# Kernel tuning notes

Hardware: AMD Instinct MI355X
Metric: run time of the kernel (lower is better)

Reference implementation:

```python
import jax, jax.numpy as jnp
import numpy as np

TEMP = 1.0
EPS = 1e-8
DIM = 1024
CODEBOOK_SIZE = 8192
N = 8192


def setup_inputs() -> dict:
    key = jax.random.key(0)
    k_h, k_cb, k_w, k_b = jax.random.split(key, 4)
    h = jax.random.normal(k_h, (N, DIM), dtype=jnp.float32)
    codebook = jax.random.normal(k_cb, (CODEBOOK_SIZE, DIM), dtype=jnp.float32)
    # RMSNorm scale initialized to ones (as in the torch module)
    scale = jnp.ones((DIM,), dtype=jnp.float32)
    # nn.Linear(dim, dim): weight [out, in], bias [out]
    bound = 1.0 / np.sqrt(DIM)
    W = jax.random.uniform(k_w, (DIM, DIM), dtype=jnp.float32, minval=-bound, maxval=bound)
    b = jax.random.uniform(k_b, (DIM,), dtype=jnp.float32, minval=-bound, maxval=bound)
    return {"h": h, "codebook": codebook, "scale": scale, "W": W, "b": b}


def reference(h, codebook, scale, W, b):
    # Squared distances via GEMM identity: ||h-c||^2 = ||h||^2 + ||c||^2 - 2 h.c
    h_sq = jnp.sum(h * h, axis=-1, keepdims=True)              # [N, 1]
    c_sq = jnp.sum(codebook * codebook, axis=-1)               # [K]
    dist = h_sq + c_sq[None, :] - 2.0 * (h @ codebook.T)       # [N, K]
    q = jax.nn.softmax(-dist / TEMP, axis=-1)                  # [N, K]
    z_e = q @ codebook                                         # [N, D]
    # residual MLP: RMSNorm then Linear
    r = h - z_e
    rms = jnp.sqrt(jnp.mean(r * r, axis=-1, keepdims=True))
    x = r / (rms + EPS) * scale
    z_q = z_e + x @ W.T + b
    return z_q
```

## Files before the change

kernel.cpp:

```cpp
#include <hip/hip_runtime.h>

typedef unsigned short u16;
typedef unsigned char u8;
typedef signed char s8;
typedef __attribute__((ext_vector_type(8))) short bf16x8;
typedef __attribute__((ext_vector_type(4))) float f32x4;
typedef __attribute__((ext_vector_type(4))) int i32x4;

__device__ __forceinline__ u16 f2bf(float x) {
  unsigned int u = __float_as_uint(x);
  u = u + 0x7FFFu + ((u >> 16) & 1u);
  return (u16)(u >> 16);
}
__device__ __forceinline__ float bf2f(u16 v) {
  return __uint_as_float(((unsigned int)v) << 16);
}

typedef const __attribute__((address_space(1))) void gas_void;
typedef __attribute__((address_space(3))) void las_void;

__device__ __forceinline__ void gld_lds16(const void* g, void* l) {
  __builtin_amdgcn_global_load_lds((gas_void*)g, (las_void*)l, 16, 0, 0);
}

#define BM 128
#define BN 128
#define BK 64
#define CAP 512
#define DU8 14

__global__ __launch_bounds__(256) void gemm_c8(
    const s8* __restrict__ A0, const s8* __restrict__ B0,
    u8* __restrict__ S, const float* __restrict__ c_sq) {
  __shared__ __align__(16) s8 lA[128 * 128];
  __shared__ __align__(16) s8 lB[128 * 128];
  int tid = threadIdx.x, wave = tid >> 6, lane = tid & 63;
  long bm = (long)blockIdx.y * 128, bn = (long)blockIdx.x * 128;
  int wm = (wave >> 1) * 64, wn = (wave & 1) * 64;
  int r15 = lane & 15, kg = lane >> 4;
  int srow = wave * 8 + (lane >> 3);
  int scol = ((lane & 7) ^ (lane >> 3)) * 16;

  i32x4 acc[4][4];
#pragma unroll
  for (int i = 0; i < 4; ++i)
#pragma unroll
    for (int j = 0; j < 4; ++j) acc[i][j] = (i32x4){0, 0, 0, 0};

  const s8* ap = A0 + bm * 1024;
  const s8* bp = B0 + bn * 1024;

  for (int k0 = 0; k0 < 1024; k0 += 128) {
    __syncthreads();
#pragma unroll
    for (int c = 0; c < 4; ++c) {
      long go = (long)(c * 32 + srow) * 1024 + k0 + scol;
      int ldoff = c * 4096 + wave * 1024;
      gld_lds16(ap + go, lA + ldoff);
      gld_lds16(bp + go, lB + ldoff);
    }
    __syncthreads();
#pragma unroll
    for (int kk = 0; kk < 2; ++kk) {
      int cb = ((kk * 4 + kg) ^ (r15 & 7)) * 16;
      i32x4 bf[4];
#pragma unroll
      for (int j = 0; j < 4; ++j)
        bf[j] = *(const i32x4*)&lB[(wn + j * 16 + r15) * 128 + cb];
#pragma unroll
      for (int i = 0; i < 4; ++i) {
        i32x4 af = *(const i32x4*)&lA[(wm + i * 16 + r15) * 128 + cb];
#pragma unroll
        for (int j = 0; j < 4; ++j)
          acc[i][j] = __builtin_amdgcn_mfma_i32_16x16x64_i8(af, bf[j], acc[i][j], 0, 0, 0);
      }
    }
  }

#pragma unroll
  for (int i = 0; i < 4; ++i) {
    long rg = bm + wm + i * 16 + kg * 4;
#pragma unroll
    for (int j = 0; j < 4; ++j) {
      long cg = bn + wn + j * 16 + r15;
      float csq = c_sq[cg];
      i32x4 m = acc[i][j];
#pragma unroll
      for (int r = 0; r < 4; ++r) {
        float v = csq - (float)m[r] * 0.0078125f;
        int q = (int)rintf((v - 1024.f) * 0.25f) + 128;
        q = q < 0 ? 0 : (q > 255 ? 255 : q);
        S[(rg + r) * 8192 + cg] = (u8)q;
      }
    }
  }
}

__device__ __forceinline__ void stage_tile(const u16* __restrict__ src, long lda,
                                           long row0, long k0, u16* ldst,
                                           int wave, int lane) {
  int srow = wave * 8 + (lane >> 3);
  int scol = ((lane & 7) ^ (lane >> 3)) * 8;
#pragma unroll
  for (int c = 0; c < 4; ++c) {
    const u16* g = src + (row0 + c * 32 + srow) * lda + k0 + scol;
    gld_lds16(g, ldst + c * 2048 + wave * 512);
  }
}

__global__ __launch_bounds__(256) void gemm_zq(
    const u16* __restrict__ A0, long lda,
    const u16* __restrict__ B0, long ldb,
    float* __restrict__ C, long ldc, int K,
    const float* __restrict__ aux0, const float* __restrict__ aux1) {
  __shared__ __align__(16) u16 lA0[BM * BK];
  __shared__ __align__(16) u16 lB0[BN * BK];

  int tid = threadIdx.x;
  int wave = tid >> 6, lane = tid & 63;
  long bm = (long)blockIdx.y * BM, bn = (long)blockIdx.x * BN;
  int wm = (wave >> 1) * 64, wn = (wave & 1) * 64;
  int r15 = lane & 15, kg = lane >> 4;

  f32x4 acc[4][4];
#pragma unroll
  for (int i = 0; i < 4; ++i)
#pragma unroll
    for (int j = 0; j < 4; ++j) acc[i][j] = (f32x4){0.f, 0.f, 0.f, 0.f};

  for (int k0 = 0; k0 < K; k0 += BK) {
    __syncthreads();
    stage_tile(A0, lda, bm, k0, lA0, wave, lane);
    stage_tile(B0, ldb, bn, k0, lB0, wave, lane);
    __syncthreads();

#pragma unroll
    for (int kk = 0; kk < 2; ++kk) {
      int cu = ((kk * 4 + kg) ^ (r15 & 7)) * 8;
      bf16x8 ah[4], bh[4];
#pragma unroll
      for (int i = 0; i < 4; ++i) {
        ah[i] = *(const bf16x8*)&lA0[(wm + i * 16 + r15) * 64 + cu];
        bh[i] = *(const bf16x8*)&lB0[(wn + i * 16 + r15) * 64 + cu];
      }
#pragma unroll
      for (int i = 0; i < 4; ++i)
#pragma unroll
        for (int j = 0; j < 4; ++j)
          acc[i][j] = __builtin_amdgcn_mfma_f32_16x16x32_bf16(ah[i], bh[j], acc[i][j], 0, 0, 0);
    }
  }

#pragma unroll
  for (int i = 0; i < 4; ++i) {
    long rg = bm + wm + i * 16 + kg * 4;
#pragma unroll
    for (int j = 0; j < 4; ++j) {
      long cg = bn + wn + j * 16 + r15;
      f32x4 v = acc[i][j];
      float bb = aux1[cg];
#pragma unroll
      for (int r = 0; r < 4; ++r)
        C[(rg + r) * ldc + cg] = v[r] + aux0[(rg + r) * ldc + cg] + bb;
    }
  }
}

__device__ __forceinline__ int q8(float x) {
  float q = rintf(x * 16.f);
  q = fminf(fmaxf(q, -127.f), 127.f);
  return (int)q;
}

__global__ __launch_bounds__(256) void prep_h_i8(const float* __restrict__ in,
                                                 s8* __restrict__ q0, int n4) {
  int i = blockIdx.x * 256 + threadIdx.x;
  if (i >= n4) return;
  float4 v = ((const float4*)in)[i];
  unsigned int w = (unsigned int)((q8(v.x) & 0xFF) | ((q8(v.y) & 0xFF) << 8) |
                                  ((q8(v.z) & 0xFF) << 16) | ((q8(v.w) & 0xFF) << 24));
  ((unsigned int*)q0)[i] = w;
}

__global__ __launch_bounds__(256) void prep_cb_i8(const float* __restrict__ cb,
                                                  s8* __restrict__ q0,
                                                  float* __restrict__ c_sq) {
  long k = blockIdx.x;
  int t = threadIdx.x, lane = t & 63, wave = t >> 6;
  float4 v = ((const float4*)(cb + k * 1024))[t];
  unsigned int w = (unsigned int)((q8(v.x) & 0xFF) | ((q8(v.y) & 0xFF) << 8) |
                                  ((q8(v.z) & 0xFF) << 16) | ((q8(v.w) & 0xFF) << 24));
  ((unsigned int*)(q0 + k * 1024))[t] = w;
  float ss = v.x * v.x + v.y * v.y + v.z * v.z + v.w * v.w;
#pragma unroll
  for (int o = 32; o; o >>= 1) ss += __shfl_xor(ss, o);
  __shared__ float sc[4];
  if (lane == 0) sc[wave] = ss;
  __syncthreads();
  if (t == 0) c_sq[k] = sc[0] + sc[1] + sc[2] + sc[3];
}

__global__ __launch_bounds__(256) void prep_bf16(const float* __restrict__ in,
                                                 u16* __restrict__ o, int n4) {
  int i = blockIdx.x * 256 + threadIdx.x;
  if (i >= n4) return;
  float4 v = ((const float4*)in)[i];
  ushort4 h;
  h.x = f2bf(v.x); h.y = f2bf(v.y); h.z = f2bf(v.z); h.w = f2bf(v.w);
  ((ushort4*)o)[i] = h;
}

__global__ __launch_bounds__(256) void scan_rows(const u8* __restrict__ S,
                                                 int* __restrict__ cand,
                                                 int* __restrict__ cnt) {
  long m = blockIdx.x;
  int t = threadIdx.x, lane = t & 63, wave = t >> 6;
  const uint4* row4 = (const uint4*)(S + m * 8192);
  uint4 va = row4[t], vb = row4[256 + t];
  unsigned int w[8] = {va.x, va.y, va.z, va.w, vb.x, vb.y, vb.z, vb.w};
  int bmin = 255;
#pragma unroll
  for (int i = 0; i < 8; ++i)
#pragma unroll
    for (int j = 0; j < 4; ++j) {
      int b = (w[i] >> (8 * j)) & 0xFF;
      bmin = b < bmin ? b : bmin;
    }
#pragma unroll
  for (int o = 32; o; o >>= 1) {
    int y = __shfl_xor(bmin, o);
    bmin = y < bmin ? y : bmin;
  }
  __shared__ int sm[4];
  __shared__ int wsum[4];
  if (lane == 0) sm[wave] = bmin;
  __syncthreads();
  bmin = min(min(sm[0], sm[1]), min(sm[2], sm[3]));
  int thr = bmin + DU8;
  int c = 0;
#pragma unroll
  for (int i = 0; i < 8; ++i)
#pragma unroll
    for (int j = 0; j < 4; ++j)
      c += (((w[i] >> (8 * j)) & 0xFF) <= (unsigned)thr);
  int pre = c;
#pragma unroll
  for (int o = 1; o < 64; o <<= 1) {
    int y = __shfl_up(pre, o);
    if (lane >= o) pre += y;
  }
  if (lane == 63) wsum[wave] = pre;
  __syncthreads();
  int base = 0;
#pragma unroll
  for (int wv = 0; wv < 4; ++wv) base += (wv < wave) ? wsum[wv] : 0;
  int pos = base + pre - c;
#pragma unroll
  for (int i = 0; i < 8; ++i)
#pragma unroll
    for (int j = 0; j < 4; ++j) {
      int b = (w[i] >> (8 * j)) & 0xFF;
      if (b <= thr) {
        int col = (i < 4 ? t * 16 : 4096 + t * 16) + (i & 3) * 4 + j;
        if (pos < CAP) cand[m * CAP + pos] = col;
        ++pos;
      }
    }
  if (t == 0) {
    int tot = wsum[0] + wsum[1] + wsum[2] + wsum[3];
    cnt[m] = tot < CAP ? tot : CAP;
  }
}

__global__ __launch_bounds__(256) void refine_rms(
    const float* __restrict__ h, const float* __restrict__ cb,
    const float* __restrict__ csq, const int* __restrict__ cand,
    const int* __restrict__ cnt, const float* __restrict__ scale,
    float* __restrict__ z_e, u16* __restrict__ x) {
  long m = blockIdx.x;
  int t = threadIdx.x, lane = t & 63, wave = t >> 6;
  int n = cnt[m];
  __shared__ float sm[4], ssum[4], sc[4];
  __shared__ float lacc[4][1024];
  const float4* h4 = (const float4*)(h + m * 1024);
  float4 hw[4];
#pragma unroll
  for (int i = 0; i < 4; ++i) hw[i] = h4[lane * 4 + i];

  float mw = -3.0e38f, sw = 0.f;
  float4 a0 = {0.f, 0.f, 0.f, 0.f}, a1 = a0, a2 = a0, a3 = a0;
  for (int j = wave; j < n; j += 4) {
    long k = cand[m * CAP + j];
    const float4* c4 = (const float4*)(cb + k * 1024);
    float4 cv0 = c4[lane * 4 + 0], cv1 = c4[lane * 4 + 1];
    float4 cv2 = c4[lane * 4 + 2], cv3 = c4[lane * 4 + 3];
    float d = hw[0].x * cv0.x + hw[0].y * cv0.y + hw[0].z * cv0.z + hw[0].w * cv0.w +
              hw[1].x * cv1.x + hw[1].y * cv1.y + hw[1].z * cv1.z + hw[1].w * cv1.w +
              hw[2].x * cv2.x + hw[2].y * cv2.y + hw[2].z * cv2.z + hw[2].w * cv2.w +
              hw[3].x * cv3.x + hw[3].y * cv3.y + hw[3].z * cv3.z + hw[3].w * cv3.w;
#pragma unroll
    for (int o = 32; o; o >>= 1) d += __shfl_xor(d, o);
    float lg = 2.f * d - csq[k];
    if (lg > mw) {
      float r = __expf(mw - lg);
      sw *= r;
      a0.x *= r; a0.y *= r; a0.z *= r; a0.w *= r;
      a1.x *= r; a1.y *= r; a1.z *= r; a1.w *= r;
      a2.x *= r; a2.y *= r; a2.z *= r; a2.w *= r;
      a3.x *= r; a3.y *= r; a3.z *= r; a3.w *= r;
      mw = lg;
    }
    float w = __expf(lg - mw);
    sw += w;
    a0.x += w * cv0.x; a0.y += w * cv0.y; a0.z += w * cv0.z; a0.w += w * cv0.w;
    a1.x += w * cv1.x; a1.y += w * cv1.y; a1.z += w * cv1.z; a1.w += w * cv1.w;
    a2.x += w * cv2.x; a2.y += w * cv2.y; a2.z += w * cv2.z; a2.w += w * cv2.w;
    a3.x += w * cv3.x; a3.y += w * cv3.y; a3.z += w * cv3.z; a3.w += w * cv3.w;
  }
  if (lane == 0) { sm[wave] = mw; ssum[wave] = sw; }
  __syncthreads();
  float M = fmaxf(fmaxf(sm[0], sm[1]), fmaxf(sm[2], sm[3]));
  float Stot = ssum[0] * __expf(sm[0] - M) + ssum[1] * __expf(sm[1] - M) +
               ssum[2] * __expf(sm[2] - M) + ssum[3] * __expf(sm[3] - M);
  float rw = __expf(mw - M);
  float* lw = &lacc[wave][lane * 16];
  *(float4*)(lw + 0) = (float4){a0.x * rw, a0.y * rw, a0.z * rw, a0.w * rw};
  *(float4*)(lw + 4) = (float4){a1.x * rw, a1.y * rw, a1.z * rw, a1.w * rw};
  *(float4*)(lw + 8) = (float4){a2.x * rw, a2.y * rw, a2.z * rw, a2.w * rw};
  *(float4*)(lw + 12) = (float4){a3.x * rw, a3.y * rw, a3.z * rw, a3.w * rw};
  __syncthreads();
  float rs = 1.f / Stot;
  float4 p0 = *(const float4*)&lacc[0][t * 4];
  float4 p1 = *(const float4*)&lacc[1][t * 4];
  float4 p2 = *(const float4*)&lacc[2][t * 4];
  float4 p3 = *(const float4*)&lacc[3][t * 4];
  float4 ze;
  ze.x = (p0.x + p1.x + p2.x + p3.x) * rs;
  ze.y = (p0.y + p1.y + p2.y + p3.y) * rs;
  ze.z = (p0.z + p1.z + p2.z + p3.z) * rs;
  ze.w = (p0.w + p1.w + p2.w + p3.w) * rs;
  *(float4*)(z_e + m * 1024 + t * 4) = ze;
  float4 hv = h4[t];
  float4 r;
  r.x = hv.x - ze.x; r.y = hv.y - ze.y; r.z = hv.z - ze.z; r.w = hv.w - ze.w;
  float ss = r.x * r.x + r.y * r.y + r.z * r.z + r.w * r.w;
#pragma unroll
  for (int o = 32; o; o >>= 1) ss += __shfl_xor(ss, o);
  if (lane == 0) sc[wave] = ss;
  __syncthreads();
  float tot = sc[0] + sc[1] + sc[2] + sc[3];
  float inv = 1.f / (sqrtf(tot * (1.f / 1024.f)) + 1e-8f);
  float4 s4 = ((const float4*)scale)[t];
  ushort4 o;
  o.x = f2bf(r.x * inv * s4.x); o.y = f2bf(r.y * inv * s4.y);
  o.z = f2bf(r.z * inv * s4.z); o.w = f2bf(r.w * inv * s4.w);
  *(ushort4*)(x + m * 1024 + t * 4) = o;
}

extern "C" void kernel_launch(void* const* d_in, const int* in_sizes, int n_in,
                              void* d_out, int out_size, void* d_ws, size_t ws_size,
                              hipStream_t stream) {
  const float* h = (const float*)d_in[0];
  const float* cb = (const float*)d_in[1];
  const float* scale = (const float*)d_in[2];
  const float* W = (const float*)d_in[3];
  const float* b = (const float*)d_in[4];
  float* out = (float*)d_out;

  char* ws = (char*)d_ws;
  size_t off = 0;
  auto alloc = [&](size_t bytes) -> char* {
    char* p = ws + off;
    off = (off + bytes + 255) & ~(size_t)255;
    return p;
  };
  s8* h8 = (s8*)alloc(8192L * 1024);
  s8* c8 = (s8*)alloc(8192L * 1024);
  u16* Wbf = (u16*)alloc(1024L * 1024 * 2);
  float* c_sq = (float*)alloc(8192L * 4);
  float* z_e = (float*)alloc(8192L * 1024 * 4);
  u16* x = (u16*)alloc(8192L * 1024 * 2);
  int* cand = (int*)alloc(8192L * CAP * 4);
  int* cnt = (int*)alloc(8192L * 4);
  u8* Sq = (u8*)alloc(8192L * 8192);

  prep_h_i8<<<8192, 256, 0, stream>>>(h, h8, 2097152);
  prep_cb_i8<<<8192, 256, 0, stream>>>(cb, c8, c_sq);
  prep_bf16<<<1024, 256, 0, stream>>>(W, Wbf, 262144);

  gemm_c8<<<dim3(64, 64), 256, 0, stream>>>(h8, c8, Sq, c_sq);
  scan_rows<<<8192, 256, 0, stream>>>(Sq, cand, cnt);
  refine_rms<<<8192, 256, 0, stream>>>(h, cb, c_sq, cand, cnt, scale, z_e, x);
  gemm_zq<<<dim3(8, 64), 256, 0, stream>>>(x, 1024L, Wbf, 1024L,
                                           out, 1024L, 1024, z_e, b);
}
```

Baseline: 219.9 us.

## Fuse row scan into refine kernel and halve gemm_zq N tile

```diff
diff --git a/kernel.cpp b/kernel.cpp
--- a/kernel.cpp
+++ b/kernel.cpp
@@ -23,9 +23,6 @@
   __builtin_amdgcn_global_load_lds((gas_void*)g, (las_void*)l, 16, 0, 0);
 }
 
-#define BM 128
-#define BN 128
-#define BK 64
 #define CAP 512
 #define DU8 14
 
@@ -96,58 +93,56 @@
   }
 }
 
-__device__ __forceinline__ void stage_tile(const u16* __restrict__ src, long lda,
-                                           long row0, long k0, u16* ldst,
-                                           int wave, int lane) {
-  int srow = wave * 8 + (lane >> 3);
-  int scol = ((lane & 7) ^ (lane >> 3)) * 8;
-#pragma unroll
-  for (int c = 0; c < 4; ++c) {
-    const u16* g = src + (row0 + c * 32 + srow) * lda + k0 + scol;
-    gld_lds16(g, ldst + c * 2048 + wave * 512);
-  }
-}
-
 __global__ __launch_bounds__(256) void gemm_zq(
     const u16* __restrict__ A0, long lda,
     const u16* __restrict__ B0, long ldb,
     float* __restrict__ C, long ldc, int K,
     const float* __restrict__ aux0, const float* __restrict__ aux1) {
-  __shared__ __align__(16) u16 lA0[BM * BK];
-  __shared__ __align__(16) u16 lB0[BN * BK];
+  __shared__ __align__(16) u16 lA0[128 * 64];
+  __shared__ __align__(16) u16 lB0[64 * 64];
 
   int tid = threadIdx.x;
   int wave = tid >> 6, lane = tid & 63;
-  long bm = (long)blockIdx.y * BM, bn = (long)blockIdx.x * BN;
-  int wm = (wave >> 1) * 64, wn = (wave & 1) * 64;
+  long bm = (long)blockIdx.y * 128, bn = (long)blockIdx.x * 64;
+  int wm = (wave >> 1) * 64, wn = (wave & 1) * 32;
   int r15 = lane & 15, kg = lane >> 4;
-
-  f32x4 acc[4][4];
+  int srow = wave * 8 + (lane >> 3);
+  int scol = ((lane & 7) ^ (lane >> 3)) * 8;
+
+  f32x4 acc[4][2];
 #pragma unroll
   for (int i = 0; i < 4; ++i)
 #pragma unroll
-    for (int j = 0; j < 4; ++j) acc[i][j] = (f32x4){0.f, 0.f, 0.f, 0.f};
-
-  for (int k0 = 0; k0 < K; k0 += BK) {
+    for (int j = 0; j < 2; ++j) acc[i][j] = (f32x4){0.f, 0.f, 0.f, 0.f};
+
+  for (int k0 = 0; k0 < K; k0 += 64) {
     __syncthreads();
-    stage_tile(A0, lda, bm, k0, lA0, wave, lane);
-    stage_tile(B0, ldb, bn, k0, lB0, wave, lane);
+#pragma unroll
+    for (int c = 0; c < 4; ++c) {
+      const u16* g = A0 + (bm + c * 32 + srow) * lda + k0 + scol;
+      gld_lds16(g, lA0 + c * 2048 + wave * 512);
+    }
+#pragma unroll
+    for (int c = 0; c < 2; ++c) {
+      const u16* g = B0 + (bn + c * 32 + srow) * ldb + k0 + scol;
+      gld_lds16(g, lB0 + c * 2048 + wave * 512);
+    }
     __syncthreads();
 
 #pragma unroll
     for (int kk = 0; kk < 2; ++kk) {
       int cu = ((kk * 4 + kg) ^ (r15 & 7)) * 8;
-      bf16x8 ah[4], bh[4];
+      bf16x8 bh[2];
+#pragma unroll
+      for (int j = 0; j < 2; ++j)
+        bh[j] = *(const bf16x8*)&lB0[(wn + j * 16 + r15) * 64 + cu];
 #pragma unroll
       for (int i = 0; i < 4; ++i) {
-        ah[i] = *(const bf16x8*)&lA0[(wm + i * 16 + r15) * 64 + cu];
-        bh[i] = *(const bf16x8*)&lB0[(wn + i * 16 + r15) * 64 + cu];
+        bf16x8 ah = *(const bf16x8*)&lA0[(wm + i * 16 + r15) * 64 + cu];
+#pragma unroll
+        for (int j = 0; j < 2; ++j)
+          acc[i][j] = __builtin_amdgcn_mfma_f32_16x16x32_bf16(ah, bh[j], acc[i][j], 0, 0, 0);
       }
-#pragma unroll
-      for (int i = 0; i < 4; ++i)
-#pragma unroll
-        for (int j = 0; j < 4; ++j)
-          acc[i][j] = __builtin_amdgcn_mfma_f32_16x16x32_bf16(ah[i], bh[j], acc[i][j], 0, 0, 0);
     }
   }
 
@@ -155,7 +150,7 @@
   for (int i = 0; i < 4; ++i) {
     long rg = bm + wm + i * 16 + kg * 4;
 #pragma unroll
-    for (int j = 0; j < 4; ++j) {
+    for (int j = 0; j < 2; ++j) {
       long cg = bn + wn + j * 16 + r15;
       f32x4 v = acc[i][j];
       float bb = aux1[cg];
@@ -210,12 +205,19 @@
   ((ushort4*)o)[i] = h;
 }
 
-__global__ __launch_bounds__(256) void scan_rows(const u8* __restrict__ S,
-                                                 int* __restrict__ cand,
-                                                 int* __restrict__ cnt) {
+__global__ __launch_bounds__(256) void refine_rms(
+    const float* __restrict__ h, const float* __restrict__ cb,
+    const float* __restrict__ csq, const u8* __restrict__ Sq,
+    const float* __restrict__ scale,
+    float* __restrict__ z_e, u16* __restrict__ x) {
   long m = blockIdx.x;
   int t = threadIdx.x, lane = t & 63, wave = t >> 6;
-  const uint4* row4 = (const uint4*)(S + m * 8192);
+  __shared__ int cand[CAP];
+  __shared__ int smi[4], wsum[4], ncand;
+  __shared__ float smf[4], ssum[4], sc[4];
+  __shared__ float lacc[4][1024];
+
+  const uint4* row4 = (const uint4*)(Sq + m * 8192);
   uint4 va = row4[t], vb = row4[256 + t];
   unsigned int w[8] = {va.x, va.y, va.z, va.w, vb.x, vb.y, vb.z, vb.w};
   int bmin = 255;
@@ -231,11 +233,9 @@
     int y = __shfl_xor(bmin, o);
     bmin = y < bmin ? y : bmin;
   }
-  __shared__ int sm[4];
-  __shared__ int wsum[4];
-  if (lane == 0) sm[wave] = bmin;
-  __syncthreads();
-  bmin = min(min(sm[0], sm[1]), min(sm[2], sm[3]));
+  if (lane == 0) smi[wave] = bmin;
+  __syncthreads();
+  bmin = min(min(smi[0], smi[1]), min(smi[2], smi[3]));
   int thr = bmin + DU8;
   int c = 0;
 #pragma unroll
@@ -262,26 +262,17 @@
       int b = (w[i] >> (8 * j)) & 0xFF;
       if (b <= thr) {
         int col = (i < 4 ? t * 16 : 4096 + t * 16) + (i & 3) * 4 + j;
-        if (pos < CAP) cand[m * CAP + pos] = col;
+        if (pos < CAP) cand[pos] = col;
         ++pos;
       }
     }
   if (t == 0) {
     int tot = wsum[0] + wsum[1] + wsum[2] + wsum[3];
-    cnt[m] = tot < CAP ? tot : CAP;
-  }
-}
-
-__global__ __launch_bounds__(256) void refine_rms(
-    const float* __restrict__ h, const float* __restrict__ cb,
-    const float* __restrict__ csq, const int* __restrict__ cand,
-    const int* __restrict__ cnt, const float* __restrict__ scale,
-    float* __restrict__ z_e, u16* __restrict__ x) {
-  long m = blockIdx.x;
-  int t = threadIdx.x, lane = t & 63, wave = t >> 6;
-  int n = cnt[m];
-  __shared__ float sm[4], ssum[4], sc[4];
-  __shared__ float lacc[4][1024];
+    ncand = tot < CAP ? tot : CAP;
+  }
+  __syncthreads();
+  int n = ncand;
+
   const float4* h4 = (const float4*)(h + m * 1024);
   float4 hw[4];
 #pragma unroll
@@ -290,7 +281,7 @@
   float mw = -3.0e38f, sw = 0.f;
   float4 a0 = {0.f, 0.f, 0.f, 0.f}, a1 = a0, a2 = a0, a3 = a0;
   for (int j = wave; j < n; j += 4) {
-    long k = cand[m * CAP + j];
+    long k = cand[j];
     const float4* c4 = (const float4*)(cb + k * 1024);
     float4 cv0 = c4[lane * 4 + 0], cv1 = c4[lane * 4 + 1];
     float4 cv2 = c4[lane * 4 + 2], cv3 = c4[lane * 4 + 3];
@@ -310,18 +301,18 @@
       a3.x *= r; a3.y *= r; a3.z *= r; a3.w *= r;
       mw = lg;
     }
-    float w = __expf(lg - mw);
-    sw += w;
-    a0.x += w * cv0.x; a0.y += w * cv0.y; a0.z += w * cv0.z; a0.w += w * cv0.w;
-    a1.x += w * cv1.x; a1.y += w * cv1.y; a1.z += w * cv1.z; a1.w += w * cv1.w;
-    a2.x += w * cv2.x; a2.y += w * cv2.y; a2.z += w * cv2.z; a2.w += w * cv2.w;
-    a3.x += w * cv3.x; a3.y += w * cv3.y; a3.z += w * cv3.z; a3.w += w * cv3.w;
-  }
-  if (lane == 0) { sm[wave] = mw; ssum[wave] = sw; }
-  __syncthreads();
-  float M = fmaxf(fmaxf(sm[0], sm[1]), fmaxf(sm[2], sm[3]));
-  float Stot = ssum[0] * __expf(sm[0] - M) + ssum[1] * __expf(sm[1] - M) +
-               ssum[2] * __expf(sm[2] - M) + ssum[3] * __expf(sm[3] - M);
+    float wgt = __expf(lg - mw);
+    sw += wgt;
+    a0.x += wgt * cv0.x; a0.y += wgt * cv0.y; a0.z += wgt * cv0.z; a0.w += wgt * cv0.w;
+    a1.x += wgt * cv1.x; a1.y += wgt * cv1.y; a1.z += wgt * cv1.z; a1.w += wgt * cv1.w;
+    a2.x += wgt * cv2.x; a2.y += wgt * cv2.y; a2.z += wgt * cv2.z; a2.w += wgt * cv2.w;
+    a3.x += wgt * cv3.x; a3.y += wgt * cv3.y; a3.z += wgt * cv3.z; a3.w += wgt * cv3.w;
+  }
+  if (lane == 0) { smf[wave] = mw; ssum[wave] = sw; }
+  __syncthreads();
+  float M = fmaxf(fmaxf(smf[0], smf[1]), fmaxf(smf[2], smf[3]));
+  float Stot = ssum[0] * __expf(smf[0] - M) + ssum[1] * __expf(smf[1] - M) +
+               ssum[2] * __expf(smf[2] - M) + ssum[3] * __expf(smf[3] - M);
   float rw = __expf(mw - M);
   float* lw = &lacc[wave][lane * 16];
   *(float4*)(lw + 0) = (float4){a0.x * rw, a0.y * rw, a0.z * rw, a0.w * rw};
@@ -380,8 +371,6 @@
   float* c_sq = (float*)alloc(8192L * 4);
   float* z_e = (float*)alloc(8192L * 1024 * 4);
   u16* x = (u16*)alloc(8192L * 1024 * 2);
-  int* cand = (int*)alloc(8192L * CAP * 4);
-  int* cnt = (int*)alloc(8192L * 4);
   u8* Sq = (u8*)alloc(8192L * 8192);
 
   prep_h_i8<<<8192, 256, 0, stream>>>(h, h8, 2097152);
@@ -389,8 +378,7 @@
   prep_bf16<<<1024, 256, 0, stream>>>(W, Wbf, 262144);
 
   gemm_c8<<<dim3(64, 64), 256, 0, stream>>>(h8, c8, Sq, c_sq);
-  scan_rows<<<8192, 256, 0, stream>>>(Sq, cand, cnt);
-  refine_rms<<<8192, 256, 0, stream>>>(h, cb, c_sq, cand, cnt, scale, z_e, x);
-  gemm_zq<<<dim3(8, 64), 256, 0, stream>>>(x, 1024L, Wbf, 1024L,
-                                           out, 1024L, 1024, z_e, b);
-}
+  refine_rms<<<8192, 256, 0, stream>>>(h, cb, c_sq, Sq, scale, z_e, x);
+  gemm_zq<<<dim3(16, 64), 256, 0, stream>>>(x, 1024L, Wbf, 1024L,
+                                            out, 1024L, 1024, z_e, b);
+}
```

New measurement: 215.9 us. About the same (-1.8%).
